# Optimization experiments

Hardware: AMD Instinct MI355X
Metric: run time of the kernel (lower is better)

Reference implementation:

```python
import jax, jax.numpy as jnp
import numpy as np

D = 256; NH = 8; NL = 4; NP = 8; DFF = 1024; NQ = 300; BS = 8
DH = D // NH
_SHAPES = np.array([[100, 100], [50, 50], [25, 25], [13, 13]], dtype=np.int64)
S = int(_SHAPES.prod(1).sum())


def setup_inputs():
    key = jax.random.key(0)
    ks = jax.random.split(key, 24)
    rn = lambda k, sh, s=0.02: jax.random.normal(k, sh, jnp.float32) * s
    lsi = np.concatenate([[0], np.cumsum(_SHAPES.prod(1))[:-1]])
    return {
        'tgt': rn(ks[0], (NQ, BS, D), 1.0),
        'tgt_query_mask': rn(ks[1], (NQ, BS, D), 1.0),
        'tgt_reference_bboxs': jax.random.uniform(ks[2], (NQ, BS, 4), jnp.float32, 0.1, 0.5),
        'tgt_reference_masks': jax.random.uniform(ks[3], (NQ, BS, 32, 32), jnp.float32),
        'memory': rn(ks[4], (S, BS, D), 1.0),
        'in_proj_w': rn(ks[5], (3 * D, D)), 'in_proj_b': jnp.zeros((3 * D,), jnp.float32),
        'out_sa_w': rn(ks[6], (D, D)), 'out_sa_b': jnp.zeros((D,), jnp.float32),
        'norm2_g': jnp.ones((D,), jnp.float32), 'norm2_b': jnp.zeros((D,), jnp.float32),
        'value_w': rn(ks[7], (D, D)), 'value_b': jnp.zeros((D,), jnp.float32),
        'off_w': rn(ks[8], (NH * NL * NP * 2, D)), 'off_b': rn(ks[9], (NH * NL * NP * 2,), 0.5),
        'aw_w': rn(ks[10], (NH * NL * NP, D)), 'aw_b': jnp.zeros((NH * NL * NP,), jnp.float32),
        'out_ca_w': rn(ks[11], (D, D)), 'out_ca_b': jnp.zeros((D,), jnp.float32),
        'norm1_g': jnp.ones((D,), jnp.float32), 'norm1_b': jnp.zeros((D,), jnp.float32),
        'lin1_w': rn(ks[12], (DFF, D)), 'lin1_b': jnp.zeros((DFF,), jnp.float32),
        'lin2_w': rn(ks[13], (D, DFF)), 'lin2_b': jnp.zeros((D,), jnp.float32),
        'norm3_g': jnp.ones((D,), jnp.float32), 'norm3_b': jnp.zeros((D,), jnp.float32),
        'memory_key_padding_mask': jnp.zeros((BS, S), bool),
        'memory_spatial_shapes': jnp.asarray(_SHAPES, jnp.int32),
        'memory_level_start_index': jnp.asarray(lsi, jnp.int32),
    }


def _lin(x, w, b):
    return x @ w.T + b


def _ln(x, g, b):
    mu = x.mean(-1, keepdims=True)
    v = ((x - mu) ** 2).mean(-1, keepdims=True)
    return (x - mu) / jnp.sqrt(v + 1e-5) * g + b


def _ms_deform(query, ref, mem, pad_mask, spatial, lstart, vw, vb, ow, ob, aww, awb, outw, outb):
    # query/ref/mem: (bs, nq, D), (bs, nq, 4 cxcywh in [0,1]), (bs, S, D)
    bs, nq, _ = query.shape
    value = _lin(mem, vw, vb)
    value = jnp.where(pad_mask[:, :, None], 0.0, value).reshape(bs, -1, NH, DH)
    off = _lin(query, ow, ob).reshape(bs, nq, NH, NL, NP, 2)
    aw = jax.nn.softmax(_lin(query, aww, awb).reshape(bs, nq, NH, NL * NP), -1)
    aw = aw.reshape(bs, nq, NH, NL, NP)
    ref6 = ref[:, :, None, None, None, :]
    loc = ref6[..., :2] + off / NP * ref6[..., 2:4] * 0.5  # (bs,nq,NH,NL,NP,2)
    Hs = spatial[:, 0].reshape(1, 1, 1, NL, 1)
    Ws = spatial[:, 1].reshape(1, 1, 1, NL, 1)
    ls = lstart.reshape(1, 1, 1, NL, 1)
    Hf = Hs.astype(jnp.float32); Wf = Ws.astype(jnp.float32)
    # grid_sample align_corners=False pixel coords
    x = loc[..., 0] * Wf - 0.5
    y = loc[..., 1] * Hf - 0.5
    x0 = jnp.floor(x); y0 = jnp.floor(y)
    vT = value.transpose(2, 0, 1, 3)  # (NH,bs,S,DH)
    acc = jnp.zeros((bs, nq, NH, NL, NP, DH), jnp.float32)
    for dx in (0.0, 1.0):
        for dy in (0.0, 1.0):
            xi = x0 + dx; yi = y0 + dy
            w = (1.0 - jnp.abs(x - xi)) * (1.0 - jnp.abs(y - yi))
            valid = ((xi >= 0) & (xi < Wf) & (yi >= 0) & (yi < Hf)).astype(jnp.float32)
            xc = jnp.clip(xi, 0.0, Wf - 1.0).astype(jnp.int32)
            yc = jnp.clip(yi, 0.0, Hf - 1.0).astype(jnp.int32)
            idx = ls + yc * Ws + xc  # flat index into S, (bs,nq,NH,NL,NP)
            iT = idx.transpose(2, 0, 1, 3, 4).reshape(NH, bs, -1)
            g = jax.vmap(lambda v, i: jnp.take_along_axis(v, i[:, :, None], axis=1))(vT, iT)
            g = g.reshape(NH, bs, nq, NL, NP, DH).transpose(1, 2, 0, 3, 4, 5)
            acc = acc + (w * valid)[..., None] * g
    out = (acc * aw[..., None]).sum(axis=(3, 4)).reshape(bs, nq, D)
    return _lin(out, outw, outb)


def reference(tgt, tgt_query_mask, tgt_reference_bboxs, tgt_reference_masks, memory,
              in_proj_w, in_proj_b, out_sa_w, out_sa_b, norm2_g, norm2_b,
              value_w, value_b, off_w, off_b, aw_w, aw_b, out_ca_w, out_ca_b,
              norm1_g, norm1_b, lin1_w, lin1_b, lin2_w, lin2_b, norm3_g, norm3_b,
              memory_key_padding_mask, memory_spatial_shapes, memory_level_start_index):
    nq, bs, _ = tgt.shape
    # --- self attention (nn.MultiheadAttention, seq-first, eval mode) ---
    q = tgt + tgt_query_mask
    qh = _lin(q, in_proj_w[:D], in_proj_b[:D]).reshape(nq, bs, NH, DH)
    kh = _lin(q, in_proj_w[D:2 * D], in_proj_b[D:2 * D]).reshape(nq, bs, NH, DH)
    vh = _lin(tgt, in_proj_w[2 * D:], in_proj_b[2 * D:]).reshape(nq, bs, NH, DH)
    logits = jnp.einsum('qbhd,kbhd->bhqk', qh, kh) / np.sqrt(DH).astype(np.float32)
    attn = jax.nn.softmax(logits, -1)
    sa = jnp.einsum('bhqk,kbhd->qbhd', attn, vh).reshape(nq, bs, D)
    sa = _lin(sa, out_sa_w, out_sa_b)
    tgt = _ln(tgt + sa, norm2_g, norm2_b)
    # --- multi-scale deformable cross attention ---
    ca = _ms_deform((tgt + tgt_query_mask).transpose(1, 0, 2),
                    tgt_reference_bboxs.transpose(1, 0, 2),
                    memory.transpose(1, 0, 2),
                    memory_key_padding_mask, memory_spatial_shapes, memory_level_start_index,
                    value_w, value_b, off_w, off_b, aw_w, aw_b, out_ca_w, out_ca_b)
    tgt = _ln(tgt + ca.transpose(1, 0, 2), norm1_g, norm1_b)
    # --- FFN ---
    t2 = _lin(jax.nn.relu(_lin(tgt, lin1_w, lin1_b)), lin2_w, lin2_b)
    return _ln(tgt + t2, norm3_g, norm3_b)
```

## Files before the change

kernel.cpp:

```cpp
#include <hip/hip_runtime.h>
#include <hip/hip_bf16.h>
#include <math.h>

#define NQ 300
#define BSZ 8
#define DIM 256
#define NHEAD 8
#define ROWS (NQ * BSZ)

typedef __attribute__((ext_vector_type(8))) short bf16x8;
typedef __attribute__((ext_vector_type(4))) float f32x4;

__device__ inline short f2bf(float f) {
  __hip_bfloat16 h = __float2bfloat16(f);
  return *reinterpret_cast<short*>(&h);
}
__device__ inline float bf2f(unsigned short u) {
  union { unsigned u; float f; } c;
  c.u = ((unsigned)u) << 16;
  return c.f;
}

__global__ __launch_bounds__(256) void add4_kernel(const float4* __restrict__ a,
                                                   const float4* __restrict__ b,
                                                   float4* __restrict__ o, int n4) {
  int i = blockIdx.x * 256 + threadIdx.x;
  if (i < n4) {
    float4 x = a[i], y = b[i];
    o[i] = make_float4(x.x + y.x, x.y + y.y, x.z + y.z, x.w + y.w);
  }
}

template <int TR>
__device__ inline void stage_tile(const float* __restrict__ g, int row0, int rmax,
                                  int stride, int k0, char* lds, int tid) {
#pragma unroll
  for (int p = 0; p < TR / 32; ++p) {
    int row = p * 32 + (tid >> 3);
    int slot = tid & 7;
    float4 v0 = make_float4(0.f, 0.f, 0.f, 0.f), v1 = v0;
    int gr = row0 + row;
    if (gr < rmax) {
      const float* s = g + (size_t)gr * stride + k0 + slot * 8;
      v0 = *(const float4*)s;
      v1 = *(const float4*)(s + 4);
    }
    bf16x8 o;
    o[0] = f2bf(v0.x); o[1] = f2bf(v0.y); o[2] = f2bf(v0.z); o[3] = f2bf(v0.w);
    o[4] = f2bf(v1.x); o[5] = f2bf(v1.y); o[6] = f2bf(v1.z); o[7] = f2bf(v1.w);
    int byte = row * 128 + slot * 16;
    byte ^= (row & 7) << 4;
    *(bf16x8*)(lds + byte) = o;
  }
}

template <int BM, int BN, bool RELU, bool VMASK, bool OBF16>
__global__ __launch_bounds__(256) void mgemm_kernel(const float* __restrict__ A,
                                                    const float* __restrict__ W,
                                                    const float* __restrict__ bias,
                                                    void* __restrict__ C, int M, int N, int K,
                                                    const unsigned char* __restrict__ vmask,
                                                    int Srows) {
  constexpr int WMT = BM / 2, WNT = BN / 2;
  constexpr int AM = WMT / 16, BF = WNT / 16;
  __shared__ char lds[(BM + BN) * 128];
  char* As = lds;
  char* Bs = lds + BM * 128;
  const int tid = threadIdx.x;
  const int lane = tid & 63;
  const int wid = tid >> 6;
  const int wr = wid >> 1, wc = wid & 1;
  const int m0 = blockIdx.x * BM, n0 = blockIdx.y * BN;

  f32x4 acc[AM][BF];
#pragma unroll
  for (int i = 0; i < AM; ++i)
#pragma unroll
    for (int j = 0; j < BF; ++j) acc[i][j] = {0.f, 0.f, 0.f, 0.f};

  const int arow0 = wr * WMT + (lane & 15);
  const int brow0 = wc * WNT + (lane & 15);
  const int lslot = (lane >> 4) * 16;

  for (int k0 = 0; k0 < K; k0 += 64) {
    __syncthreads();
    stage_tile<BM>(A, m0, M, K, k0, As, tid);
    stage_tile<BN>(W, n0, N, K, k0, Bs, tid);
    __syncthreads();
#pragma unroll
    for (int kk = 0; kk < 2; ++kk) {
      bf16x8 af[AM], bfr[BF];
#pragma unroll
      for (int i = 0; i < AM; ++i) {
        int row = arow0 + i * 16;
        int byte = row * 128 + kk * 64 + lslot;
        byte ^= (row & 7) << 4;
        af[i] = *(bf16x8*)(As + byte);
      }
#pragma unroll
      for (int j = 0; j < BF; ++j) {
        int row = brow0 + j * 16;
        int byte = row * 128 + kk * 64 + lslot;
        byte ^= (row & 7) << 4;
        bfr[j] = *(bf16x8*)(Bs + byte);
      }
#pragma unroll
      for (int i = 0; i < AM; ++i)
#pragma unroll
        for (int j = 0; j < BF; ++j)
          acc[i][j] = __builtin_amdgcn_mfma_f32_16x16x32_bf16(af[i], bfr[j], acc[i][j], 0, 0, 0);
    }
  }

  const int colbase = n0 + wc * WNT + (lane & 15);
  const int rowq = (lane >> 4) * 4;
#pragma unroll
  for (int i = 0; i < AM; ++i) {
#pragma unroll
    for (int r = 0; r < 4; ++r) {
      int grow = m0 + wr * WMT + i * 16 + rowq + r;
      if (grow >= M) continue;
      float mfac = 1.f;
      if (VMASK) mfac = vmask[(size_t)(grow & 7) * Srows + (grow >> 3)] ? 0.f : 1.f;
#pragma unroll
      for (int j = 0; j < BF; ++j) {
        int col = colbase + j * 16;
        float v = acc[i][j][r] + bias[col];
        if (VMASK) v *= mfac;
        if (RELU) v = fmaxf(v, 0.f);
        if (OBF16)
          ((__hip_bfloat16*)C)[(size_t)grow * N + col] = __float2bfloat16(v);
        else
          ((float*)C)[(size_t)grow * N + col] = v;
      }
    }
  }
}

__global__ __launch_bounds__(256) void attn_kernel(const float* __restrict__ cqk,
                                                   const float* __restrict__ cv,
                                                   float* __restrict__ out) {
  __shared__ float Ks[NQ][32];
  __shared__ float Vs[NQ][32];
  const int b = blockIdx.x, h = blockIdx.y, qt = blockIdx.z;
  const int tid = threadIdx.x;
  for (int i = tid; i < NQ * 8; i += 256) {
    int qi = i >> 3, c4 = (i & 7) * 4;
    *(float4*)&Ks[qi][c4] = *(const float4*)&cqk[((size_t)(qi * 8 + b)) * 512 + 256 + h * 32 + c4];
    *(float4*)&Vs[qi][c4] = *(const float4*)&cv[((size_t)(qi * 8 + b)) * 256 + h * 32 + c4];
  }
  __syncthreads();
  const int row = qt * 64 + (tid >> 2);
  const int qr = tid & 3;
  if (row >= NQ) return;
  float qv[8];
  const float* qptr = &cqk[((size_t)(row * 8 + b)) * 512 + h * 32 + qr * 8];
  *(float4*)&qv[0] = *(const float4*)&qptr[0];
  *(float4*)&qv[4] = *(const float4*)&qptr[4];
  const float scale = 0.17677669529663687f;
  float m = -3.0e38f, l = 0.f;
  float acc[8] = {0.f, 0.f, 0.f, 0.f, 0.f, 0.f, 0.f, 0.f};
  for (int k = 0; k < NQ; ++k) {
    const float* kr = &Ks[k][qr * 8];
    float p = 0.f;
#pragma unroll
    for (int j = 0; j < 8; ++j) p = fmaf(qv[j], kr[j], p);
    p += __shfl_xor(p, 1, 4);
    p += __shfl_xor(p, 2, 4);
    float s = p * scale;
    float mn = fmaxf(m, s);
    float corr = __expf(m - mn);
    float e = __expf(s - mn);
    l = l * corr + e;
    const float* vr = &Vs[k][qr * 8];
#pragma unroll
    for (int j = 0; j < 8; ++j) acc[j] = fmaf(acc[j], corr, e * vr[j]);
    m = mn;
  }
  float inv = 1.f / l;
  float* op = &out[((size_t)(row * 8 + b)) * 256 + h * 32 + qr * 8];
#pragma unroll
  for (int j = 0; j < 8; ++j) op[j] = acc[j] * inv;
}

__global__ __launch_bounds__(256) void resid_ln_kernel(const float* __restrict__ X,
                                                       const float* __restrict__ R,
                                                       const float* __restrict__ g,
                                                       const float* __restrict__ be,
                                                       const float* __restrict__ addmask,
                                                       float* __restrict__ out,
                                                       float* __restrict__ out2) {
  const int r = blockIdx.x, c = threadIdx.x;
  const size_t i = (size_t)r * 256 + c;
  float x = X[i] + R[i];
  float s = x;
#pragma unroll
  for (int o = 32; o; o >>= 1) s += __shfl_xor(s, o, 64);
  __shared__ float sm[4], sv[4];
  const int w = c >> 6;
  if ((c & 63) == 0) sm[w] = s;
  __syncthreads();
  float mu = (sm[0] + sm[1] + sm[2] + sm[3]) * (1.f / 256.f);
  float d = x - mu;
  float v = d * d;
#pragma unroll
  for (int o = 32; o; o >>= 1) v += __shfl_xor(v, o, 64);
  if ((c & 63) == 0) sv[w] = v;
  __syncthreads();
  float var = (sv[0] + sv[1] + sv[2] + sv[3]) * (1.f / 256.f);
  float y = d * (1.f / sqrtf(var + 1e-5f)) * g[c] + be[c];
  out[i] = y;
  if (out2) out2[i] = y + addmask[i];
}

__global__ __launch_bounds__(256) void deform_kernel(const unsigned short* __restrict__ value,
                                                     const float* __restrict__ off,
                                                     const float* __restrict__ awl,
                                                     const float* __restrict__ bbox,
                                                     const int* __restrict__ spatial,
                                                     const int* __restrict__ lstart,
                                                     float* __restrict__ out, int S) {
  __shared__ int sH[4], sW[4], sL[4];
  __shared__ float sbb[4];
  const int r = blockIdx.x;
  const int b = r & 7;
  const int tid = threadIdx.x;
  if (tid < 4) {
    sH[tid] = spatial[tid * 2];
    sW[tid] = spatial[tid * 2 + 1];
    sL[tid] = lstart[tid];
    sbb[tid] = bbox[(size_t)r * 4 + tid];
  }
  __syncthreads();
  const float cx = sbb[0], cy = sbb[1], bw = sbb[2], bh = sbb[3];
  float ox = off[(size_t)r * 512 + (size_t)tid * 2];
  float oy = off[(size_t)r * 512 + (size_t)tid * 2 + 1];
  float a = awl[(size_t)r * 256 + tid];
  float mx = a;
#pragma unroll
  for (int o = 16; o; o >>= 1) mx = fmaxf(mx, __shfl_xor(mx, o, 32));
  float e = __expf(a - mx);
  float ssum = e;
#pragma unroll
  for (int o = 16; o; o >>= 1) ssum += __shfl_xor(ssum, o, 32);
  float myaw = e / ssum;

  float acc = 0.f;
  const size_t vb = (size_t)b * 256 + (size_t)tid;
  for (int lp = 0; lp < 32; ++lp) {
    const int l = lp >> 3;
    float bx = __shfl(ox, lp, 32);
    float by = __shfl(oy, lp, 32);
    float alp = __shfl(myaw, lp, 32);
    const float Wf = (float)sW[l], Hf = (float)sH[l];
    const int ls = sL[l], Wi = sW[l];
    float lx = cx + bx * 0.0625f * bw;
    float ly = cy + by * 0.0625f * bh;
    float x = lx * Wf - 0.5f;
    float y = ly * Hf - 0.5f;
    float x0 = floorf(x), y0 = floorf(y);
    float fx = x - x0, fy = y - y0;
    float tap = 0.f;
#pragma unroll
    for (int t = 0; t < 4; ++t) {
      float xi = x0 + (float)(t & 1);
      float yi = y0 + (float)(t >> 1);
      if (xi >= 0.f && yi >= 0.f && xi < Wf && yi < Hf) {
        float wx = (t & 1) ? fx : (1.f - fx);
        float wy = (t >> 1) ? fy : (1.f - fy);
        int idx = ls + (int)yi * Wi + (int)xi;
        tap = fmaf(wx * wy, bf2f(value[(size_t)idx * 2048 + vb]), tap);
      }
    }
    acc = fmaf(alp, tap, acc);
  }
  out[(size_t)r * 256 + tid] = acc;
}

extern "C" void kernel_launch(void* const* d_in, const int* in_sizes, int n_in, void* d_out,
                              int out_size, void* d_ws, size_t ws_size, hipStream_t stream) {
  (void)n_in; (void)out_size; (void)ws_size;
  const float* tgt = (const float*)d_in[0];
  const float* qmask = (const float*)d_in[1];
  const float* bbox = (const float*)d_in[2];
  const float* memory = (const float*)d_in[4];
  const float* ipw = (const float*)d_in[5];
  const float* ipb = (const float*)d_in[6];
  const float* osw = (const float*)d_in[7];
  const float* osb = (const float*)d_in[8];
  const float* n2g = (const float*)d_in[9];
  const float* n2b = (const float*)d_in[10];
  const float* vw = (const float*)d_in[11];
  const float* vbi = (const float*)d_in[12];
  const float* ow = (const float*)d_in[13];
  const float* ob = (const float*)d_in[14];
  const float* aww = (const float*)d_in[15];
  const float* awb = (const float*)d_in[16];
  const float* ocw = (const float*)d_in[17];
  const float* ocb = (const float*)d_in[18];
  const float* n1g = (const float*)d_in[19];
  const float* n1b = (const float*)d_in[20];
  const float* l1w = (const float*)d_in[21];
  const float* l1b = (const float*)d_in[22];
  const float* l2w = (const float*)d_in[23];
  const float* l2b = (const float*)d_in[24];
  const float* n3g = (const float*)d_in[25];
  const float* n3b = (const float*)d_in[26];
  const unsigned char* kpmask = (const unsigned char*)d_in[27];
  const int* spatial = (const int*)d_in[28];
  const int* lstart = (const int*)d_in[29];
  float* out = (float*)d_out;

  const int S = in_sizes[4] / (BSZ * DIM);
  const int Mv = S * BSZ;

  float* ws = (float*)d_ws;
  size_t o = 0;
  unsigned short* value = (unsigned short*)(ws + o); o += (size_t)Mv * DIM / 2;
  float* qsum = ws + o; o += (size_t)ROWS * DIM;
  float* cqk = ws + o; o += (size_t)ROWS * 512;
  float* cv = ws + o; o += (size_t)ROWS * DIM;
  float* sraw = ws + o; o += (size_t)ROWS * DIM;
  float* proj = ws + o; o += (size_t)ROWS * DIM;
  float* tgt2 = ws + o; o += (size_t)ROWS * DIM;
  float* q2 = ws + o; o += (size_t)ROWS * DIM;
  float* tgt3 = ws + o; o += (size_t)ROWS * DIM;
  float* ffn1 = ws + o; o += (size_t)ROWS * 1024;

  const int MB = (ROWS + 63) / 64;

  add4_kernel<<<dim3((ROWS * DIM / 4 + 255) / 256), 256, 0, stream>>>(
      (const float4*)tgt, (const float4*)qmask, (float4*)qsum, ROWS * DIM / 4);
  mgemm_kernel<64, 64, false, false, false><<<dim3(MB, 8), 256, 0, stream>>>(
      qsum, ipw, ipb, cqk, ROWS, 512, DIM, nullptr, 0);
  mgemm_kernel<64, 64, false, false, false><<<dim3(MB, 4), 256, 0, stream>>>(
      tgt, ipw + 512 * DIM, ipb + 512, cv, ROWS, 256, DIM, nullptr, 0);
  attn_kernel<<<dim3(BSZ, NHEAD, (NQ + 63) / 64), 256, 0, stream>>>(cqk, cv, sraw);
  mgemm_kernel<64, 64, false, false, false><<<dim3(MB, 4), 256, 0, stream>>>(
      sraw, osw, osb, proj, ROWS, 256, DIM, nullptr, 0);
  resid_ln_kernel<<<ROWS, 256, 0, stream>>>(proj, tgt, n2g, n2b, qmask, tgt2, q2);
  mgemm_kernel<128, 128, false, true, true><<<dim3((Mv + 127) / 128, 2), 256, 0, stream>>>(
      memory, vw, vbi, value, Mv, 256, DIM, kpmask, S);
  mgemm_kernel<64, 64, false, false, false><<<dim3(MB, 8), 256, 0, stream>>>(
      q2, ow, ob, cqk, ROWS, 512, DIM, nullptr, 0);
  mgemm_kernel<64, 64, false, false, false><<<dim3(MB, 4), 256, 0, stream>>>(
      q2, aww, awb, cv, ROWS, 256, DIM, nullptr, 0);
  deform_kernel<<<ROWS, 256, 0, stream>>>(value, cqk, cv, bbox, spatial, lstart, sraw, S);
  mgemm_kernel<64, 64, false, false, false><<<dim3(MB, 4), 256, 0, stream>>>(
      sraw, ocw, ocb, proj, ROWS, 256, DIM, nullptr, 0);
  resid_ln_kernel<<<ROWS, 256, 0, stream>>>(proj, tgt2, n1g, n1b, nullptr, tgt3, nullptr);
  mgemm_kernel<64, 64, true, false, false><<<dim3(MB, 16), 256, 0, stream>>>(
      tgt3, l1w, l1b, ffn1, ROWS, 1024, DIM, nullptr, 0);
  mgemm_kernel<64, 64, false, false, false><<<dim3(MB, 4), 256, 0, stream>>>(
      ffn1, l2w, l2b, proj, ROWS, 256, 1024, nullptr, 0);
  resid_ln_kernel<<<ROWS, 256, 0, stream>>>(proj, tgt3, n3g, n3b, nullptr, out, nullptr);
}
```

Measured before the change: 495.2 us.

## Pre-convert weights to swizzled bf16 tiles and load A directly into registers

Adds a single pre-pass kernel that converts all weight matrices to bf16, laid out as 64-row by 256-K swizzled chunks. The GEMM then bulk-copies each weight chunk into LDS with plain vector loads. Activation (A) tiles no longer go through LDS: each lane reads fp32 rows from global memory and converts them to bf16 in registers. The grid now runs N-blocks along x, so blocks that share a weight tile are adjacent, and the weights are converted once per call instead of once per block. The cost is an extra conversion launch every call and uncoalesced, unshared global reads of A that are repeated for each N block.

```diff
diff --git a/kernel.cpp b/kernel.cpp
--- a/kernel.cpp
+++ b/kernel.cpp
@@ -31,100 +31,126 @@
   }
 }
 
-template <int TR>
-__device__ inline void stage_tile(const float* __restrict__ g, int row0, int rmax,
-                                  int stride, int k0, char* lds, int tid) {
-#pragma unroll
-  for (int p = 0; p < TR / 32; ++p) {
-    int row = p * 32 + (tid >> 3);
-    int slot = tid & 7;
-    float4 v0 = make_float4(0.f, 0.f, 0.f, 0.f), v1 = v0;
-    int gr = row0 + row;
-    if (gr < rmax) {
-      const float* s = g + (size_t)gr * stride + k0 + slot * 8;
-      v0 = *(const float4*)s;
-      v1 = *(const float4*)(s + 4);
-    }
-    bf16x8 o;
-    o[0] = f2bf(v0.x); o[1] = f2bf(v0.y); o[2] = f2bf(v0.z); o[3] = f2bf(v0.w);
-    o[4] = f2bf(v1.x); o[5] = f2bf(v1.y); o[6] = f2bf(v1.z); o[7] = f2bf(v1.w);
-    int byte = row * 128 + slot * 16;
-    byte ^= (row & 7) << 4;
-    *(bf16x8*)(lds + byte) = o;
-  }
-}
-
-template <int BM, int BN, bool RELU, bool VMASK, bool OBF16>
-__global__ __launch_bounds__(256) void mgemm_kernel(const float* __restrict__ A,
-                                                    const float* __restrict__ W,
-                                                    const float* __restrict__ bias,
-                                                    void* __restrict__ C, int M, int N, int K,
-                                                    const unsigned char* __restrict__ vmask,
-                                                    int Srows) {
-  constexpr int WMT = BM / 2, WNT = BN / 2;
-  constexpr int AM = WMT / 16, BF = WNT / 16;
-  __shared__ char lds[(BM + BN) * 128];
-  char* As = lds;
-  char* Bs = lds + BM * 128;
-  const int tid = threadIdx.x;
-  const int lane = tid & 63;
-  const int wid = tid >> 6;
+struct WEntry {
+  const float* src;
+  unsigned short* dst;
+  int K;
+  int gstart;
+};
+struct WPack {
+  WEntry e[8];
+  int total;
+};
+__global__ __launch_bounds__(256) void wconv_kernel(WPack P) {
+  int g = blockIdx.x * 256 + threadIdx.x;
+  if (g >= P.total) return;
+  int i = 0;
+  while (i < 7 && g >= P.e[i + 1].gstart) ++i;
+  const float* src = P.e[i].src;
+  unsigned short* dst = P.e[i].dst;
+  const int K = P.e[i].K;
+  int gl = g - P.e[i].gstart;
+  int gpr = K >> 3;
+  int r = gl / gpr, gk = gl - r * gpr;
+  int nb = r >> 6, rr = r & 63;
+  int c = gk >> 5, gi = gk & 31;
+  const float* s = src + (size_t)r * K + gk * 8;
+  float4 v0 = *(const float4*)s, v1 = *(const float4*)(s + 4);
+  bf16x8 o;
+  o[0] = f2bf(v0.x); o[1] = f2bf(v0.y); o[2] = f2bf(v0.z); o[3] = f2bf(v0.w);
+  o[4] = f2bf(v1.x); o[5] = f2bf(v1.y); o[6] = f2bf(v1.z); o[7] = f2bf(v1.w);
+  size_t byte = ((size_t)(nb * (K >> 8) + c) * 64 + rr) * 512 + ((gi * 16) ^ ((rr & 7) << 4));
+  *(bf16x8*)((char*)dst + byte) = o;
+}
+
+template <int BM, bool RELU, bool VMASK, bool OBF16>
+__global__ __launch_bounds__(256) void mgemm2(const float* __restrict__ A,
+                                              const unsigned short* __restrict__ Wz,
+                                              const float* __restrict__ bias,
+                                              void* __restrict__ C, int M, int N, int K,
+                                              const unsigned char* __restrict__ vmask,
+                                              int Srows) {
+  constexpr int WMT = BM / 2;
+  constexpr int AM = WMT / 16;
+  __shared__ char Bs[32768];
+  const int tid = threadIdx.x, lane = tid & 63, wid = tid >> 6;
   const int wr = wid >> 1, wc = wid & 1;
-  const int m0 = blockIdx.x * BM, n0 = blockIdx.y * BN;
-
-  f32x4 acc[AM][BF];
+  const int nb = blockIdx.x;
+  const int m0 = blockIdx.y * BM;
+  const int l15 = lane & 15, lk = lane >> 4;
+
+  f32x4 acc[AM][2];
 #pragma unroll
   for (int i = 0; i < AM; ++i)
 #pragma unroll
-    for (int j = 0; j < BF; ++j) acc[i][j] = {0.f, 0.f, 0.f, 0.f};
-
-  const int arow0 = wr * WMT + (lane & 15);
-  const int brow0 = wc * WNT + (lane & 15);
-  const int lslot = (lane >> 4) * 16;
-
-  for (int k0 = 0; k0 < K; k0 += 64) {
+    for (int j = 0; j < 2; ++j) acc[i][j] = {0.f, 0.f, 0.f, 0.f};
+
+  const int nchunk = K >> 8;
+  const unsigned short* wt = Wz + (size_t)nb * nchunk * 16384;
+
+  const float* aptr[AM];
+#pragma unroll
+  for (int i = 0; i < AM; ++i) {
+    int row = m0 + wr * WMT + i * 16 + l15;
+    if (row > M - 1) row = M - 1;
+    aptr[i] = A + (size_t)row * K + lk * 8;
+  }
+
+  int bbyte[2];
+#pragma unroll
+  for (int j = 0; j < 2; ++j) {
+    int rr = wc * 32 + j * 16 + l15;
+    bbyte[j] = rr * 512 + ((lk * 16) ^ ((rr & 7) << 4));
+  }
+  const int swzmask = 0;
+
+  for (int c = 0; c < nchunk; ++c) {
     __syncthreads();
-    stage_tile<BM>(A, m0, M, K, k0, As, tid);
-    stage_tile<BN>(W, n0, N, K, k0, Bs, tid);
+    const float4* src = (const float4*)(wt + c * 16384);
+#pragma unroll
+    for (int i = 0; i < 8; ++i) ((float4*)Bs)[tid + i * 256] = src[tid + i * 256];
     __syncthreads();
 #pragma unroll
-    for (int kk = 0; kk < 2; ++kk) {
-      bf16x8 af[AM], bfr[BF];
+    for (int s = 0; s < 8; ++s) {
+      bf16x8 af[AM], bfr[2];
 #pragma unroll
       for (int i = 0; i < AM; ++i) {
-        int row = arow0 + i * 16;
-        int byte = row * 128 + kk * 64 + lslot;
-        byte ^= (row & 7) << 4;
-        af[i] = *(bf16x8*)(As + byte);
+        const float* p = aptr[i] + c * 256 + s * 32;
+        float4 v0 = *(const float4*)p, v1 = *(const float4*)(p + 4);
+        bf16x8 o;
+        o[0] = f2bf(v0.x); o[1] = f2bf(v0.y); o[2] = f2bf(v0.z); o[3] = f2bf(v0.w);
+        o[4] = f2bf(v1.x); o[5] = f2bf(v1.y); o[6] = f2bf(v1.z); o[7] = f2bf(v1.w);
+        af[i] = o;
       }
 #pragma unroll
-      for (int j = 0; j < BF; ++j) {
-        int row = brow0 + j * 16;
-        int byte = row * 128 + kk * 64 + lslot;
-        byte ^= (row & 7) << 4;
+      for (int j = 0; j < 2; ++j) {
+        int rr = wc * 32 + j * 16 + l15;
+        int g = s * 4 + lk;
+        int byte = rr * 512 + ((g * 16) ^ ((rr & 7) << 4));
         bfr[j] = *(bf16x8*)(Bs + byte);
       }
+      (void)swzmask;
+      (void)bbyte;
 #pragma unroll
       for (int i = 0; i < AM; ++i)
 #pragma unroll
-        for (int j = 0; j < BF; ++j)
+        for (int j = 0; j < 2; ++j)
           acc[i][j] = __builtin_amdgcn_mfma_f32_16x16x32_bf16(af[i], bfr[j], acc[i][j], 0, 0, 0);
     }
   }
 
-  const int colbase = n0 + wc * WNT + (lane & 15);
-  const int rowq = (lane >> 4) * 4;
+  const int colb = nb * 64 + wc * 32 + l15;
 #pragma unroll
   for (int i = 0; i < AM; ++i) {
 #pragma unroll
     for (int r = 0; r < 4; ++r) {
-      int grow = m0 + wr * WMT + i * 16 + rowq + r;
+      int grow = m0 + wr * WMT + i * 16 + lk * 4 + r;
       if (grow >= M) continue;
       float mfac = 1.f;
       if (VMASK) mfac = vmask[(size_t)(grow & 7) * Srows + (grow >> 3)] ? 0.f : 1.f;
 #pragma unroll
-      for (int j = 0; j < BF; ++j) {
-        int col = colbase + j * 16;
+      for (int j = 0; j < 2; ++j) {
+        int col = colb + j * 16;
         float v = acc[i][j][r] + bias[col];
         if (VMASK) v *= mfac;
         if (RELU) v = fmaxf(v, 0.f);
@@ -326,32 +352,58 @@
   float* q2 = ws + o; o += (size_t)ROWS * DIM;
   float* tgt3 = ws + o; o += (size_t)ROWS * DIM;
   float* ffn1 = ws + o; o += (size_t)ROWS * 1024;
+  unsigned short* wz = (unsigned short*)(ws + o);
+  unsigned short* ipw_z = wz;
+  unsigned short* osw_z = ipw_z + 768 * 256;
+  unsigned short* vw_z  = osw_z + 256 * 256;
+  unsigned short* ow_z  = vw_z + 256 * 256;
+  unsigned short* aww_z = ow_z + 512 * 256;
+  unsigned short* ocw_z = aww_z + 256 * 256;
+  unsigned short* l1w_z = ocw_z + 256 * 256;
+  unsigned short* l2w_z = l1w_z + 1024 * 256;
+
+  WPack P;
+  int gs = 0;
+  auto ent = [&](int idx, const float* s, unsigned short* d, int N_, int K_) {
+    P.e[idx] = {s, d, K_, gs};
+    gs += N_ * K_ / 8;
+  };
+  ent(0, ipw, ipw_z, 768, 256);
+  ent(1, osw, osw_z, 256, 256);
+  ent(2, vw, vw_z, 256, 256);
+  ent(3, ow, ow_z, 512, 256);
+  ent(4, aww, aww_z, 256, 256);
+  ent(5, ocw, ocw_z, 256, 256);
+  ent(6, l1w, l1w_z, 1024, 256);
+  ent(7, l2w, l2w_z, 256, 1024);
+  P.total = gs;
+  wconv_kernel<<<dim3((gs + 255) / 256), 256, 0, stream>>>(P);
 
   const int MB = (ROWS + 63) / 64;
 
   add4_kernel<<<dim3((ROWS * DIM / 4 + 255) / 256), 256, 0, stream>>>(
       (const float4*)tgt, (const float4*)qmask, (float4*)qsum, ROWS * DIM / 4);
-  mgemm_kernel<64, 64, false, false, false><<<dim3(MB, 8), 256, 0, stream>>>(
-      qsum, ipw, ipb, cqk, ROWS, 512, DIM, nullptr, 0);
-  mgemm_kernel<64, 64, false, false, false><<<dim3(MB, 4), 256, 0, stream>>>(
-      tgt, ipw + 512 * DIM, ipb + 512, cv, ROWS, 256, DIM, nullptr, 0);
+  mgemm2<64, false, false, false><<<dim3(8, MB), 256, 0, stream>>>(
+      qsum, ipw_z, ipb, cqk, ROWS, 512, DIM, nullptr, 0);
+  mgemm2<64, false, false, false><<<dim3(4, MB), 256, 0, stream>>>(
+      tgt, ipw_z + 8 * 16384, ipb + 512, cv, ROWS, 256, DIM, nullptr, 0);
   attn_kernel<<<dim3(BSZ, NHEAD, (NQ + 63) / 64), 256, 0, stream>>>(cqk, cv, sraw);
-  mgemm_kernel<64, 64, false, false, false><<<dim3(MB, 4), 256, 0, stream>>>(
-      sraw, osw, osb, proj, ROWS, 256, DIM, nullptr, 0);
+  mgemm2<64, false, false, false><<<dim3(4, MB), 256, 0, stream>>>(
+      sraw, osw_z, osb, proj, ROWS, 256, DIM, nullptr, 0);
   resid_ln_kernel<<<ROWS, 256, 0, stream>>>(proj, tgt, n2g, n2b, qmask, tgt2, q2);
-  mgemm_kernel<128, 128, false, true, true><<<dim3((Mv + 127) / 128, 2), 256, 0, stream>>>(
-      memory, vw, vbi, value, Mv, 256, DIM, kpmask, S);
-  mgemm_kernel<64, 64, false, false, false><<<dim3(MB, 8), 256, 0, stream>>>(
-      q2, ow, ob, cqk, ROWS, 512, DIM, nullptr, 0);
-  mgemm_kernel<64, 64, false, false, false><<<dim3(MB, 4), 256, 0, stream>>>(
-      q2, aww, awb, cv, ROWS, 256, DIM, nullptr, 0);
+  mgemm2<128, false, true, true><<<dim3(4, (Mv + 127) / 128), 256, 0, stream>>>(
+      memory, vw_z, vbi, value, Mv, 256, DIM, kpmask, S);
+  mgemm2<64, false, false, false><<<dim3(8, MB), 256, 0, stream>>>(
+      q2, ow_z, ob, cqk, ROWS, 512, DIM, nullptr, 0);
+  mgemm2<64, false, false, false><<<dim3(4, MB), 256, 0, stream>>>(
+      q2, aww_z, awb, cv, ROWS, 256, DIM, nullptr, 0);
   deform_kernel<<<ROWS, 256, 0, stream>>>(value, cqk, cv, bbox, spatial, lstart, sraw, S);
-  mgemm_kernel<64, 64, false, false, false><<<dim3(MB, 4), 256, 0, stream>>>(
-      sraw, ocw, ocb, proj, ROWS, 256, DIM, nullptr, 0);
+  mgemm2<64, false, false, false><<<dim3(4, MB), 256, 0, stream>>>(
+      sraw, ocw_z, ocb, proj, ROWS, 256, DIM, nullptr, 0);
   resid_ln_kernel<<<ROWS, 256, 0, stream>>>(proj, tgt2, n1g, n1b, nullptr, tgt3, nullptr);
-  mgemm_kernel<64, 64, true, false, false><<<dim3(MB, 16), 256, 0, stream>>>(
-      tgt3, l1w, l1b, ffn1, ROWS, 1024, DIM, nullptr, 0);
-  mgemm_kernel<64, 64, false, false, false><<<dim3(MB, 4), 256, 0, stream>>>(
-      ffn1, l2w, l2b, proj, ROWS, 256, 1024, nullptr, 0);
+  mgemm2<64, true, false, false><<<dim3(16, MB), 256, 0, stream>>>(
+      tgt3, l1w_z, l1b, ffn1, ROWS, 1024, DIM, nullptr, 0);
+  mgemm2<64, false, false, false><<<dim3(4, MB), 256, 0, stream>>>(
+      ffn1, l2w_z, l2b, proj, ROWS, 256, 1024, nullptr, 0);
   resid_ln_kernel<<<ROWS, 256, 0, stream>>>(proj, tgt3, n3g, n3b, nullptr, out, nullptr);
 }
```

Measured after the change: 553.7 us. +11.8%, slower.
